# Optimization experiments

Measured on AMD Instinct MI355X. Metric: run time of the kernel, lower is better.

Reference implementation:

```python
import jax, jax.numpy as jnp
import numpy as np

B, U, D, H = 8, 256, 512, 32

def _layernorm(x, g, b, eps=1e-5):
    m = jnp.mean(x, axis=-1, keepdims=True)
    v = jnp.var(x, axis=-1, keepdims=True)
    return (x - m) * jax.lax.rsqrt(v + eps) * g + b

def setup_inputs() -> dict:
    key = jax.random.key(0)
    ks = jax.random.split(key, 12)
    s = 0.02
    return {
        "z_dyn": jax.random.normal(ks[0], (B, U, D), jnp.float32),
        "z_sem": jax.random.normal(ks[1], (B, U, D), jnp.float32),
        "te_w": jax.random.normal(ks[2], (H, D), jnp.float32) * s,
        "w_ih": jax.random.normal(ks[3], (3 * D, D), jnp.float32) * s,
        "w_hh": jax.random.normal(ks[4], (3 * D, D), jnp.float32) * s,
        "b_ih": jnp.zeros((3 * D,), jnp.float32),
        "b_hh": jnp.zeros((3 * D,), jnp.float32),
        "ln_g": jnp.ones((D,), jnp.float32),
        "ln_b": jnp.zeros((D,), jnp.float32),
        "ln2_g": jnp.ones((2 * D,), jnp.float32),
        "ln2_b": jnp.zeros((2 * D,), jnp.float32),
        "w1": jax.random.normal(ks[5], (D, 2 * D), jnp.float32) * s,
        "b1": jnp.zeros((D,), jnp.float32),
        "w2": jax.random.normal(ks[6], (D, D), jnp.float32) * s,
        "b2": jnp.zeros((D,), jnp.float32),
        "horizon": H,
    }

def reference(z_dyn, z_sem, te_w, w_ih, w_hh, b_ih, b_hh, ln_g, ln_b,
              ln2_g, ln2_b, w1, b1, w2, b2, horizon):
    b, u, d = z_dyn.shape
    h0 = z_dyn.reshape(b * u, d)
    sem = z_sem.reshape(b * u, d)
    idx = jnp.minimum(jnp.arange(horizon), te_w.shape[0] - 1)
    ts = te_w[idx]  # [horizon, d]

    def step(h, t):
        x = sem + t
        gi = x @ w_ih.T + b_ih   # [bu, 3d]
        gh = h @ w_hh.T + b_hh
        ir, iz, inn = jnp.split(gi, 3, axis=-1)
        hr, hz, hn = jnp.split(gh, 3, axis=-1)
        r = jax.nn.sigmoid(ir + hr)
        z = jax.nn.sigmoid(iz + hz)
        n = jnp.tanh(inn + r * hn)
        h_new = (1.0 - z) * n + z * h
        h_norm = _layernorm(h_new, ln_g, ln_b)
        cat = jnp.concatenate([sem, h_norm], axis=-1)
        hid = jax.nn.gelu(_layernorm(cat, ln2_g, ln2_b) @ w1.T + b1,
                          approximate=False)
        sem_h = sem + hid @ w2.T + b2
        return h_new, (h_norm, sem_h)

    _, (dyn, sems) = jax.lax.scan(step, h0, ts)  # [horizon, bu, d]
    dyn = dyn.reshape(horizon, b, u, d).transpose(1, 2, 0, 3)
    sems = sems.reshape(horizon, b, u, d).transpose(1, 2, 0, 3)
    return dyn, sems
```

## Files before the change

kernel.cpp:

```cpp
#include <hip/hip_runtime.h>
#include <math.h>


typedef unsigned short u16;
using bf16x8 = __attribute__((ext_vector_type(8))) short;
using f32x4  = __attribute__((ext_vector_type(4))) float;

#define DEV __device__ __forceinline__

constexpr int D   = 512;
constexpr int D3  = 1536;
constexpr int H   = 32;
constexpr int BU  = 2048;
constexpr long long OUT_HALF = (long long)BU * H * D;

DEV u16 f2bf(float x){
  union { float f; unsigned u; } c; c.f = x;
  unsigned u = c.u;
  u += 0x7fffu + ((u >> 16) & 1u);
  return (u16)(u >> 16);
}
DEV float bf2f(u16 b){
  union { unsigned u; float f; } c; c.u = ((unsigned)b) << 16; return c.f;
}

DEV void gload_lds16(const void* g, void* l){
  __builtin_amdgcn_global_load_lds(
      (const __attribute__((address_space(1))) void*)g,
      (__attribute__((address_space(3))) void*)l, 16, 0, 0);
}

DEV f32x4 mfma16(bf16x8 a, bf16x8 b, f32x4 c){
  return __builtin_amdgcn_mfma_f32_16x16x32_bf16(a, b, c, 0, 0, 0);
}

DEV float fsigm(float x){ return 1.f / (1.f + __expf(-x)); }
DEV float ftanh(float x){ return 1.f - 2.f / (1.f + __expf(2.f * x)); }

__global__ __launch_bounds__(256) void prep_kernel(
    const float* __restrict__ z_dyn, const float* __restrict__ z_sem,
    const float* __restrict__ te_w,  const float* __restrict__ w_ih,
    const float* __restrict__ w_hh,  const float* __restrict__ ln_g,
    const float* __restrict__ ln_b,  const float* __restrict__ ln2_g,
    const float* __restrict__ ln2_b, const float* __restrict__ w1,
    const float* __restrict__ b1,    const float* __restrict__ w2,
    float* __restrict__ h1, u16* __restrict__ hbh2, u16* __restrict__ hbl2,
    u16* __restrict__ sem_hi, u16* __restrict__ sem_lo,
    u16* __restrict__ wih_hi, u16* __restrict__ wih_lo,
    u16* __restrict__ whh_hi, u16* __restrict__ whh_lo,
    u16* __restrict__ W1s, u16* __restrict__ W1g, u16* __restrict__ w2bf,
    float* __restrict__ c1, float* __restrict__ c2p,
    float* __restrict__ d1, float* __restrict__ d2, float* __restrict__ Tg)
{
  int i = blockIdx.x * 256 + threadIdx.x;
  if (i < BU * D) {
    float hv = z_dyn[i];
    h1[i] = hv;
    u16 hh = f2bf(hv);
    hbh2[i] = hh;
    hbl2[i] = f2bf(hv - bf2f(hh));
    float sv = z_sem[i];
    u16 sh_ = f2bf(sv);
    sem_hi[i] = sh_;
    sem_lo[i] = f2bf(sv - bf2f(sh_));
  }
  if (i < D3 * D) {
    float wv = w_ih[i];
    u16 wh = f2bf(wv);
    wih_hi[i] = wh;
    wih_lo[i] = f2bf(wv - bf2f(wh));
    float uv = w_hh[i];
    u16 uh = f2bf(uv);
    whh_hi[i] = uh;
    whh_lo[i] = f2bf(uv - bf2f(uh));
  }
  if (i < D * D) {
    int k = i >> 9, j = i & 511;
    W1s[i]  = f2bf(w1[k * 1024 + j] * ln2_g[j]);
    w2bf[i] = f2bf(w2[i]);
  }
  if (i < D * 64) {
    int r = i >> 6, ln = i & 63;
    float sc1 = 0.f, sc2 = 0.f, sd1 = 0.f, sd2 = 0.f;
    #pragma unroll
    for (int jj = 0; jj < 8; ++jj) {
      int j = jj * 64 + ln;
      float wA = w1[r * 1024 + j];
      float wB = w1[r * 1024 + 512 + j];
      sc1 += wA * ln2_g[j] + wB * ln2_g[512 + j];
      sc2 += wA * ln2_b[j] + wB * ln2_b[512 + j];
      float wBg = wB * ln2_g[512 + j];
      float wg = wBg * ln_g[j];
      sd1 += wg;
      sd2 += wBg * ln_b[j];
      W1g[r * 512 + j] = f2bf(wg);
    }
    #pragma unroll
    for (int o = 1; o < 64; o <<= 1) {
      sc1 += __shfl_xor(sc1, o); sc2 += __shfl_xor(sc2, o);
      sd1 += __shfl_xor(sd1, o); sd2 += __shfl_xor(sd2, o);
    }
    if (ln == 0) {
      c1[r] = sc1;
      c2p[r] = sc2 + b1[r];
      d1[r] = sd1;
      d2[r] = sd2;
    }
  }
  if (i < H * D3) {
    int c = i >> 5, t = i & 31;
    float s = 0.f;
    for (int d0 = 0; d0 < D; ++d0) s += te_w[t * D + d0] * w_ih[c * D + d0];
    Tg[t * D3 + c] = s;
  }
}

__global__ __launch_bounds__(256) void rowstats_kernel(
    const float* __restrict__ sem, float* __restrict__ Ssem,
    float* __restrict__ Ssem2)
{
  const int wid = threadIdx.x >> 6, lane = threadIdx.x & 63;
  const int row = blockIdx.x * 4 + wid;
  const float* p = sem + (size_t)row * D + lane * 8;
  float4 a0 = *(const float4*)p;
  float4 a1 = *(const float4*)(p + 4);
  float s  = a0.x + a0.y + a0.z + a0.w + a1.x + a1.y + a1.z + a1.w;
  float s2 = a0.x*a0.x + a0.y*a0.y + a0.z*a0.z + a0.w*a0.w
           + a1.x*a1.x + a1.y*a1.y + a1.z*a1.z + a1.w*a1.w;
  #pragma unroll
  for (int o = 1; o < 64; o <<= 1) { s += __shfl_xor(s, o); s2 += __shfl_xor(s2, o); }
  if (lane == 0) { Ssem[row] = s; Ssem2[row] = s2; }
}

__global__ __launch_bounds__(256) void setup_kernel(
    const u16* __restrict__ sem_hi, const u16* __restrict__ sem_lo,
    const u16* __restrict__ wih_hi, const u16* __restrict__ wih_lo,
    const u16* __restrict__ W1s, float* __restrict__ G0,
    float* __restrict__ Psem, const float* __restrict__ b_ih)
{
  __shared__ __align__(16) char smem[32768];
  char* Ah = smem;
  char* Al = smem + 8192;
  char* Bh = smem + 16384;
  char* Bl = smem + 24576;
  const int tid = threadIdx.x, wid = tid >> 6, lane = tid & 63;
  const int wr = wid >> 1, wc = wid & 1;
  const bool isG0 = blockIdx.y < 24;
  const u16* Bsrc = isG0 ? wih_hi : W1s;
  const int row0 = blockIdx.x * 64;
  const int col0 = (isG0 ? blockIdx.y : blockIdx.y - 24) * 64;

  f32x4 acc[2][2] = {};
  for (int kt = 0; kt < 8; ++kt) {
    #pragma unroll
    for (int it = 0; it < 2; ++it) {
      int s = it * 256 + tid, pr = s >> 3, pc = s & 7;
      int lch = pc ^ (pr & 7);
      size_t aoff = (size_t)(row0 + pr) * D + kt * 64 + lch * 8;
      size_t boff = (size_t)(col0 + pr) * D + kt * 64 + lch * 8;
      gload_lds16(sem_hi + aoff, Ah + it * 4096 + wid * 1024);
      gload_lds16(Bsrc + boff,   Bh + it * 4096 + wid * 1024);
      if (isG0) {
        gload_lds16(sem_lo + aoff, Al + it * 4096 + wid * 1024);
        gload_lds16(wih_lo + boff, Bl + it * 4096 + wid * 1024);
      }
    }
    asm volatile("s_waitcnt vmcnt(0)" ::: "memory");
    __syncthreads();

    const int lc = lane & 15, hi2 = lane >> 4;
    #pragma unroll
    for (int kk = 0; kk < 2; ++kk) {
      int ch = kk * 4 + hi2;
      bf16x8 afh[2], afl[2], bfh[2], bfl[2];
      #pragma unroll
      for (int mi = 0; mi < 2; ++mi) {
        int r = wr * 32 + mi * 16 + lc;
        int o = r * 128 + ((ch ^ (r & 7)) << 4);
        afh[mi] = *(const bf16x8*)(Ah + o);
        if (isG0) afl[mi] = *(const bf16x8*)(Al + o);
      }
      #pragma unroll
      for (int ci = 0; ci < 2; ++ci) {
        int r = wc * 32 + ci * 16 + lc;
        int o = r * 128 + ((ch ^ (r & 7)) << 4);
        bfh[ci] = *(const bf16x8*)(Bh + o);
        if (isG0) bfl[ci] = *(const bf16x8*)(Bl + o);
      }
      #pragma unroll
      for (int mi = 0; mi < 2; ++mi)
        #pragma unroll
        for (int ci = 0; ci < 2; ++ci) {
          f32x4 a = acc[mi][ci];
          a = mfma16(afh[mi], bfh[ci], a);
          if (isG0) {
            a = mfma16(afl[mi], bfh[ci], a);
            a = mfma16(afh[mi], bfl[ci], a);
          }
          acc[mi][ci] = a;
        }
    }
    __syncthreads();
  }
  const int lj = lane >> 4, lc2 = lane & 15;
  #pragma unroll
  for (int mi = 0; mi < 2; ++mi)
    #pragma unroll
    for (int ci = 0; ci < 2; ++ci)
      #pragma unroll
      for (int j = 0; j < 4; ++j) {
        int row = row0 + wr * 32 + mi * 16 + lj * 4 + j;
        int col = col0 + wc * 32 + ci * 16 + lc2;
        float v = acc[mi][ci][j];
        if (isG0) G0[(size_t)row * D3 + col] = v + b_ih[col];
        else      Psem[(size_t)row * D + col] = v;
      }
}

__global__ __launch_bounds__(256, 4) void fused_kernel(
    int t,
    const u16* __restrict__ hbh_in, const u16* __restrict__ hbl_in,
    u16* __restrict__ hbh_out, u16* __restrict__ hbl_out,
    const float* __restrict__ hf_in, float* __restrict__ hf_out,
    const u16* __restrict__ whh_hi, const u16* __restrict__ whh_lo,
    const float* __restrict__ G0, const float* __restrict__ Tg,
    const float* __restrict__ bhh,
    float4* __restrict__ stats_w, float* __restrict__ dyn,
    const float* __restrict__ ln_g, const float* __restrict__ ln_b,
    const float* __restrict__ Ssem, const float* __restrict__ Ssem2,
    const u16* __restrict__ lbh,
    const float4* __restrict__ stats_r, const u16* __restrict__ W1g,
    const float* __restrict__ Psem, const float* __restrict__ d1,
    const float* __restrict__ d2, const float* __restrict__ c1,
    const float* __restrict__ c2p, u16* __restrict__ hid_w,
    const u16* __restrict__ hid_r, const u16* __restrict__ w2bf,
    const float* __restrict__ zsem, const float* __restrict__ b2,
    float* __restrict__ sems)
{
  __shared__ __align__(16) char smem[32768];
  const int bid = blockIdx.x;
  const int tid = threadIdx.x, wid = tid >> 6, lane = tid & 63;
  const int wr = wid >> 1, wc = wid & 1;
  const int lc = lane & 15, hi2 = lane >> 4;
  const int lj = lane >> 4, lc2 = lane & 15;

  if (bid < 512) {
    if (t >= H) return;
    const int row0 = (bid & 31) * 64;
    const int gc   = (bid >> 5) * 32;
    char* Ah = smem;
    char* Al = smem + 8192;
    char* Bh = smem + 16384;
    char* Bl = smem + 28672;
    f32x4 acc[3][2] = {};

    const int gcol = gc + wc * 16 + lc2;

    float pre_gr[2][4], pre_gz[2][4], pre_gn[2][4], pre_hf[2][4];
    #pragma unroll
    for (int mi = 0; mi < 2; ++mi)
      #pragma unroll
      for (int j = 0; j < 4; ++j) {
        int row = row0 + wr * 32 + mi * 16 + lj * 4 + j;
        size_t g0i = (size_t)row * D3 + gcol;
        pre_gr[mi][j] = G0[g0i];
        pre_gz[mi][j] = G0[g0i + 512];
        pre_gn[mi][j] = G0[g0i + 1024];
        pre_hf[mi][j] = hf_in[(size_t)row * D + gcol];
      }

    for (int kt = 0; kt < 8; ++kt) {
      #pragma unroll
      for (int it = 0; it < 2; ++it) {
        int s = it * 256 + tid, pr = s >> 3, pc = s & 7;
        int lch = pc ^ (pr & 7);
        size_t off = (size_t)(row0 + pr) * D + kt * 64 + lch * 8;
        gload_lds16(hbh_in + off, Ah + it * 4096 + wid * 1024);
        gload_lds16(hbl_in + off, Al + it * 4096 + wid * 1024);
      }
      #pragma unroll
      for (int it = 0; it < 3; ++it) {
        int s = it * 256 + tid, pr = s >> 3, pc = s & 7;
        int lch = pc ^ (pr & 7);
        int g = pr >> 5, lr = pr & 31;
        gload_lds16(whh_hi + (size_t)(g * D + gc + lr) * D + kt * 64 + lch * 8,
                    Bh + it * 4096 + wid * 1024);
      }
      {
        int pr = tid >> 3, pc = tid & 7;
        int lch = pc ^ (pr & 7);
        gload_lds16(whh_lo + (size_t)(2 * D + gc + pr) * D + kt * 64 + lch * 8,
                    Bl + wid * 1024);
      }
      asm volatile("s_waitcnt vmcnt(0)" ::: "memory");
      __syncthreads();

      #pragma unroll
      for (int kk = 0; kk < 2; ++kk) {
        int ch = kk * 4 + hi2;
        bf16x8 afh[2], afl[2];
        #pragma unroll
        for (int mi = 0; mi < 2; ++mi) {
          int r = wr * 32 + mi * 16 + lc;
          int o = r * 128 + ((ch ^ (r & 7)) << 4);
          afh[mi] = *(const bf16x8*)(Ah + o);
          afl[mi] = *(const bf16x8*)(Al + o);
        }
        const int rloc = wc * 16 + lc;
        #pragma unroll
        for (int g = 0; g < 3; ++g) {
          int rb = g * 32 + rloc;
          int bo = rb * 128 + ((ch ^ (rb & 7)) << 4);
          bf16x8 bh = *(const bf16x8*)(Bh + bo);
          #pragma unroll
          for (int mi = 0; mi < 2; ++mi) {
            f32x4 a = acc[g][mi];
            a = mfma16(afh[mi], bh, a);
            a = mfma16(afl[mi], bh, a);
            acc[g][mi] = a;
          }
        }
        {
          int bo = rloc * 128 + ((ch ^ (rloc & 7)) << 4);
          bf16x8 bl = *(const bf16x8*)(Bl + bo);
          #pragma unroll
          for (int mi = 0; mi < 2; ++mi)
            acc[2][mi] = mfma16(afh[mi], bl, acc[2][mi]);
        }
      }
      __syncthreads();
    }

    const float br = bhh[gcol];
    const float bz = bhh[512 + gcol];
    const float bn = bhh[1024 + gcol];
    const float tr = Tg[t * D3 + gcol];
    const float tz = Tg[t * D3 + 512 + gcol];
    const float tn = Tg[t * D3 + 1024 + gcol];
    #pragma unroll
    for (int mi = 0; mi < 2; ++mi)
      #pragma unroll
      for (int j = 0; j < 4; ++j) {
        int row = row0 + wr * 32 + mi * 16 + lj * 4 + j;
        float gr = pre_gr[mi][j] + tr + acc[0][mi][j];
        float gz = pre_gz[mi][j] + tz + acc[1][mi][j];
        float gn = pre_gn[mi][j] + tn;
        float r = fsigm(gr + br);
        float z = fsigm(gz + bz);
        float n = ftanh(gn + r * (acc[2][mi][j] + bn));
        size_t hi_ = (size_t)row * D + gcol;
        float hnew = (1.f - z) * n + z * pre_hf[mi][j];
        hf_out[hi_] = hnew;
        u16 hh = f2bf(hnew);
        hbh_out[hi_] = hh;
        hbl_out[hi_] = f2bf(hnew - bf2f(hh));
      }
  } else if (bid < 768) {
    if (t < 2 || t > H + 1) return;
    const int i = bid - 512;
    const int row0 = (i & 31) * 64, col0 = (i >> 5) * 64;
    char* bufp[2] = { smem, smem + 16384 };
    f32x4 acc[2][2] = {};

    float pre_ps[2][2][4];
    float4 pre_st[2][4];
    #pragma unroll
    for (int mi = 0; mi < 2; ++mi)
      #pragma unroll
      for (int j = 0; j < 4; ++j) {
        int row = row0 + wr * 32 + mi * 16 + lj * 4 + j;
        pre_st[mi][j] = stats_r[row];
        #pragma unroll
        for (int ci = 0; ci < 2; ++ci) {
          int col = col0 + wc * 32 + ci * 16 + lc2;
          pre_ps[mi][ci][j] = Psem[(size_t)row * D + col];
        }
      }

    auto stage = [&](char* base, int kt){
      #pragma unroll
      for (int it = 0; it < 2; ++it) {
        int s = it * 256 + tid, pr = s >> 3, pc = s & 7;
        int lch = pc ^ (pr & 7);
        gload_lds16(lbh + (size_t)(row0 + pr) * D + kt * 64 + lch * 8,
                    base + it * 4096 + wid * 1024);
        gload_lds16(W1g + (size_t)(col0 + pr) * D + kt * 64 + lch * 8,
                    base + 8192 + it * 4096 + wid * 1024);
      }
    };

    stage(bufp[0], 0);
    __syncthreads();
    int buf = 0;
    for (int kt = 0; kt < 8; ++kt) {
      if (kt < 7) stage(bufp[buf ^ 1], kt + 1);
      const char* Ah = bufp[buf];
      const char* Bs = bufp[buf] + 8192;
      #pragma unroll
      for (int kk = 0; kk < 2; ++kk) {
        int ch = kk * 4 + hi2;
        bf16x8 afh[2], bf[2];
        #pragma unroll
        for (int mi = 0; mi < 2; ++mi) {
          int r = wr * 32 + mi * 16 + lc;
          afh[mi] = *(const bf16x8*)(Ah + r * 128 + ((ch ^ (r & 7)) << 4));
        }
        #pragma unroll
        for (int ci = 0; ci < 2; ++ci) {
          int r = wc * 32 + ci * 16 + lc;
          bf[ci] = *(const bf16x8*)(Bs + r * 128 + ((ch ^ (r & 7)) << 4));
        }
        #pragma unroll
        for (int mi = 0; mi < 2; ++mi)
          #pragma unroll
          for (int ci = 0; ci < 2; ++ci)
            acc[mi][ci] = mfma16(afh[mi], bf[ci], acc[mi][ci]);
      }
      __syncthreads();
      buf ^= 1;
    }

    #pragma unroll
    for (int mi = 0; mi < 2; ++mi)
      #pragma unroll
      for (int ci = 0; ci < 2; ++ci)
        #pragma unroll
        for (int j = 0; j < 4; ++j) {
          int row = row0 + wr * 32 + mi * 16 + lj * 4 + j;
          int col = col0 + wc * 32 + ci * 16 + lc2;
          float4 st = pre_st[mi][j];
          float hn_w1 = st.x * acc[mi][ci][j] - st.y * d1[col] + d2[col];
          float pre = st.z * (pre_ps[mi][ci][j] + hn_w1)
                      - st.w * c1[col] + c2p[col];
          float gl = 0.5f * pre * (1.f + erff(pre * 0.70710678118654752f));
          hid_w[(size_t)row * D + col] = f2bf(gl);
        }
  } else if (bid < 1024) {
    if (t < 3) return;
    const int ts = t - 3;
    const int i = bid - 768;
    const int row0 = (i & 31) * 64, col0 = (i >> 5) * 64;
    char* bufp[2] = { smem, smem + 16384 };
    f32x4 acc[2][2] = {};

    float pre_zs[2][2][4];
    #pragma unroll
    for (int mi = 0; mi < 2; ++mi)
      #pragma unroll
      for (int ci = 0; ci < 2; ++ci)
        #pragma unroll
        for (int j = 0; j < 4; ++j) {
          int row = row0 + wr * 32 + mi * 16 + lj * 4 + j;
          int col = col0 + wc * 32 + ci * 16 + lc2;
          pre_zs[mi][ci][j] = zsem[(size_t)row * D + col];
        }

    auto stage = [&](char* base, int kt){
      #pragma unroll
      for (int it = 0; it < 2; ++it) {
        int s = it * 256 + tid, pr = s >> 3, pc = s & 7;
        int lch = pc ^ (pr & 7);
        gload_lds16(hid_r + (size_t)(row0 + pr) * D + kt * 64 + lch * 8,
                    base + it * 4096 + wid * 1024);
        gload_lds16(w2bf + (size_t)(col0 + pr) * D + kt * 64 + lch * 8,
                    base + 8192 + it * 4096 + wid * 1024);
      }
    };

    stage(bufp[0], 0);
    __syncthreads();
    int buf = 0;
    for (int kt = 0; kt < 8; ++kt) {
      if (kt < 7) stage(bufp[buf ^ 1], kt + 1);
      const char* As = bufp[buf];
      const char* Bs = bufp[buf] + 8192;
      #pragma unroll
      for (int kk = 0; kk < 2; ++kk) {
        int ch = kk * 4 + hi2;
        bf16x8 af[2], bf[2];
        #pragma unroll
        for (int mi = 0; mi < 2; ++mi) {
          int r = wr * 32 + mi * 16 + lc;
          af[mi] = *(const bf16x8*)(As + r * 128 + ((ch ^ (r & 7)) << 4));
        }
        #pragma unroll
        for (int ci = 0; ci < 2; ++ci) {
          int r = wc * 32 + ci * 16 + lc;
          bf[ci] = *(const bf16x8*)(Bs + r * 128 + ((ch ^ (r & 7)) << 4));
        }
        #pragma unroll
        for (int mi = 0; mi < 2; ++mi)
          #pragma unroll
          for (int ci = 0; ci < 2; ++ci)
            acc[mi][ci] = mfma16(af[mi], bf[ci], acc[mi][ci]);
      }
      __syncthreads();
      buf ^= 1;
    }

    #pragma unroll
    for (int mi = 0; mi < 2; ++mi)
      #pragma unroll
      for (int ci = 0; ci < 2; ++ci)
        #pragma unroll
        for (int j = 0; j < 4; ++j) {
          int row = row0 + wr * 32 + mi * 16 + lj * 4 + j;
          int col = col0 + wc * 32 + ci * 16 + lc2;
          float v = pre_zs[mi][ci][j] + acc[mi][ci][j] + b2[col];
          __builtin_nontemporal_store(
              v, &sems[((size_t)row * H + ts) * D + col]);
        }
  } else {
    if (t < 1 || t > H) return;
    const int tt = t - 1;
    const int base = (bid - 1024) * 16 + wid * 4;
    const float4 g0 = *(const float4*)(ln_g + lane * 8);
    const float4 g1 = *(const float4*)(ln_g + lane * 8 + 4);
    const float4 b0 = *(const float4*)(ln_b + lane * 8);
    const float4 b1v = *(const float4*)(ln_b + lane * 8 + 4);
    const float gg[8] = {g0.x,g0.y,g0.z,g0.w,g1.x,g1.y,g1.z,g1.w};
    const float bb[8] = {b0.x,b0.y,b0.z,b0.w,b1v.x,b1v.y,b1v.z,b1v.w};

    for (int rr = 0; rr < 4; ++rr) {
      const int row = base + rr;
      const float* hp = hf_in + (size_t)row * D + lane * 8;
      float4 a0 = *(const float4*)hp, a1 = *(const float4*)(hp + 4);
      float h[8] = {a0.x, a0.y, a0.z, a0.w, a1.x, a1.y, a1.z, a1.w};
      float s1 = 0.f;
      #pragma unroll
      for (int k = 0; k < 8; ++k) s1 += h[k];
      #pragma unroll
      for (int o = 1; o < 64; o <<= 1) s1 += __shfl_xor(s1, o);
      float m1 = s1 * (1.f / 512.f);
      float s2 = 0.f;
      #pragma unroll
      for (int k = 0; k < 8; ++k) {
        float dv = h[k] - m1;
        s2 += dv * dv;
      }
      #pragma unroll
      for (int o = 1; o < 64; o <<= 1) s2 += __shfl_xor(s2, o);
      float rsd1 = rsqrtf(s2 * (1.f / 512.f) + 1e-5f);

      float hn[8];
      float sh = 0.f, sh2 = 0.f;
      #pragma unroll
      for (int k = 0; k < 8; ++k) {
        float x = (h[k] - m1) * rsd1 * gg[k] + bb[k];
        hn[k] = x; sh += x; sh2 += x * x;
      }
      float* dp = dyn + ((size_t)row * H + tt) * D + lane * 8;
      f32x4 v0 = {hn[0], hn[1], hn[2], hn[3]};
      f32x4 v1 = {hn[4], hn[5], hn[6], hn[7]};
      __builtin_nontemporal_store(v0, (f32x4*)dp);
      __builtin_nontemporal_store(v1, (f32x4*)(dp + 4));

      #pragma unroll
      for (int o = 1; o < 64; o <<= 1) {
        sh += __shfl_xor(sh, o); sh2 += __shfl_xor(sh2, o);
      }
      if (lane == 0) {
        float m2 = (Ssem[row] + sh) * (1.f / 1024.f);
        float vv = (Ssem2[row] + sh2) * (1.f / 1024.f) - m2 * m2;
        float rs2 = rsqrtf(vv + 1e-5f);
        stats_w[row] = make_float4(rsd1, m1 * rsd1, rs2, m2 * rs2);
      }
    }
  }
}

extern "C" void kernel_launch(void* const* d_in, const int* in_sizes, int n_in,
                              void* d_out, int out_size, void* d_ws, size_t ws_size,
                              hipStream_t stream)
{
  (void)in_sizes; (void)n_in; (void)out_size; (void)ws_size;
  const float* z_dyn = (const float*)d_in[0];
  const float* z_sem = (const float*)d_in[1];
  const float* te_w  = (const float*)d_in[2];
  const float* w_ih  = (const float*)d_in[3];
  const float* w_hh  = (const float*)d_in[4];
  const float* b_ih  = (const float*)d_in[5];
  const float* b_hh  = (const float*)d_in[6];
  const float* ln_g  = (const float*)d_in[7];
  const float* ln_b  = (const float*)d_in[8];
  const float* ln2_g = (const float*)d_in[9];
  const float* ln2_b = (const float*)d_in[10];
  const float* w1    = (const float*)d_in[11];
  const float* b1    = (const float*)d_in[12];
  const float* w2    = (const float*)d_in[13];
  const float* b2    = (const float*)d_in[14];

  char* ws = (char*)d_ws;
  const size_t MB = 1ull << 20;
  u16* hbh[3] = { (u16*)(ws + 0),      (u16*)(ws + 2 * MB),  (u16*)(ws + 4 * MB) };
  u16* hbl[3] = { (u16*)(ws + 6 * MB), (u16*)(ws + 8 * MB),  (u16*)(ws + 10 * MB) };
  float* G0     = (float*)(ws + 12 * MB);
  float* Psem   = (float*)(ws + 25 * MB);
  u16*  sem_hi  = (u16*)(ws + 29 * MB);
  u16*  sem_lo  = (u16*)(ws + 31 * MB);
  u16*  hid0    = (u16*)(ws + 33 * MB);
  u16*  hid1    = (u16*)(ws + 35 * MB);
  u16*  wih_hi  = (u16*)(ws + 37 * MB);
  u16*  wih_lo  = (u16*)(ws + 37 * MB + 1572864);
  u16*  whh_hi  = (u16*)(ws + 40 * MB);
  u16*  whh_lo  = (u16*)(ws + 40 * MB + 1572864);
  u16*  W1s     = (u16*)(ws + 43 * MB);
  u16*  W1g     = (u16*)(ws + 43 * MB + 524288);
  u16*  w2bf    = (u16*)(ws + 44 * MB);
  float* c1     = (float*)(ws + 45 * MB);
  float* c2p    = (float*)(ws + 45 * MB + 16384);
  float* d1     = (float*)(ws + 45 * MB + 32768);
  float* d2     = (float*)(ws + 45 * MB + 49152);
  float* Ssem   = (float*)(ws + 45 * MB + 65536);
  float* Ssem2  = (float*)(ws + 45 * MB + 81920);
  float4* stats0 = (float4*)(ws + 46 * MB);
  float4* stats1 = (float4*)(ws + 46 * MB + 32768);
  float* Tg     = (float*)(ws + 47 * MB);
  float* hf0    = (float*)(ws + 48 * MB);
  float* hf1    = (float*)(ws + 52 * MB);

  float* outp = (float*)d_out;
  float* out_dyn  = outp;
  float* out_sems = outp + OUT_HALF;

  prep_kernel<<<4096, 256, 0, stream>>>(
      z_dyn, z_sem, te_w, w_ih, w_hh, ln_g, ln_b, ln2_g, ln2_b, w1, b1, w2,
      hf1, hbh[2], hbl[2], sem_hi, sem_lo, wih_hi, wih_lo, whh_hi, whh_lo,
      W1s, W1g, w2bf, c1, c2p, d1, d2, Tg);
  rowstats_kernel<<<512, 256, 0, stream>>>(z_sem, Ssem, Ssem2);
  setup_kernel<<<dim3(32, 32), 256, 0, stream>>>(
      sem_hi, sem_lo, wih_hi, wih_lo, W1s, G0, Psem, b_ih);

  for (int t = 0; t <= H + 2; ++t) {
    int s_out  = ((t % 3) + 3) % 3;
    int s_in   = (((t - 1) % 3) + 3) % 3;
    int s_ln   = (((t - 2) % 3) + 3) % 3;
    float* hf_out      = (t & 1) ? hf1 : hf0;
    const float* hf_in = (t & 1) ? hf0 : hf1;
    float4* st_w = ((t - 1) & 1) ? stats1 : stats0;
    const float4* st_r = ((t - 2) & 1) ? stats1 : stats0;
    u16* hidw = ((t - 2) & 1) ? hid1 : hid0;
    const u16* hidr = ((t - 3) & 1) ? hid1 : hid0;

    fused_kernel<<<dim3(1152), dim3(256), 0, stream>>>(
        t,
        hbh[s_in], hbl[s_in], hbh[s_out], hbl[s_out],
        hf_in, hf_out,
        whh_hi, whh_lo, G0, Tg, b_hh,
        st_w, out_dyn, ln_g, ln_b, Ssem, Ssem2,
        hbh[s_ln], st_r, W1g, Psem, d1, d2, c1, c2p, hidw,
        hidr, w2bf, z_sem, b2, out_sems);
  }
}
```

Before: 722.4 us.

## Double-buffer the recurrent GEMM K-loop with async LDS prefetch

Splits the K loop of the hidden-state GEMM into 16 steps of 32 columns and alternates between two 16KB LDS buffers. The loads for step kt+2 are issued right after step kt's compute, and a partial vmcnt wait lets global loads overlap MFMA work. The swizzle is reworked to fit the 64-byte row halves. This costs twice as many barriers and smaller per-step compute, and it depends on vmcnt counting being exact.

```diff
diff --git a/kernel.cpp b/kernel.cpp
--- a/kernel.cpp
+++ b/kernel.cpp
@@ -248,10 +248,8 @@
     if (t >= H) return;
     const int row0 = (bid & 31) * 64;
     const int gc   = (bid >> 5) * 32;
-    char* Ah = smem;
-    char* Al = smem + 8192;
-    char* Bh = smem + 16384;
-    char* Bl = smem + 28672;
+    char* b0 = smem;
+    char* b1 = smem + 16384;
     f32x4 acc[3][2] = {};
 
     const int gcol = gc + wc * 16 + lc2;
@@ -269,66 +267,72 @@
         pre_hf[mi][j] = hf_in[(size_t)row * D + gcol];
       }
 
-    for (int kt = 0; kt < 8; ++kt) {
+    auto stage = [&](char* base, int kt){
+      { int row = tid >> 2;
+        int ko = kt * 32 + (((tid & 3) ^ ((tid >> 3) & 3)) << 3);
+        size_t off = (size_t)(row0 + row) * D + ko;
+        gload_lds16(hbh_in + off, base + wid * 1024);
+        gload_lds16(hbl_in + off, base + 4096 + wid * 1024);
+      }
       #pragma unroll
       for (int it = 0; it < 2; ++it) {
-        int s = it * 256 + tid, pr = s >> 3, pc = s & 7;
-        int lch = pc ^ (pr & 7);
-        size_t off = (size_t)(row0 + pr) * D + kt * 64 + lch * 8;
-        gload_lds16(hbh_in + off, Ah + it * 4096 + wid * 1024);
-        gload_lds16(hbl_in + off, Al + it * 4096 + wid * 1024);
-      }
-      #pragma unroll
-      for (int it = 0; it < 3; ++it) {
-        int s = it * 256 + tid, pr = s >> 3, pc = s & 7;
-        int lch = pc ^ (pr & 7);
-        int g = pr >> 5, lr = pr & 31;
-        gload_lds16(whh_hi + (size_t)(g * D + gc + lr) * D + kt * 64 + lch * 8,
-                    Bh + it * 4096 + wid * 1024);
-      }
-      {
-        int pr = tid >> 3, pc = tid & 7;
-        int lch = pc ^ (pr & 7);
-        gload_lds16(whh_lo + (size_t)(2 * D + gc + pr) * D + kt * 64 + lch * 8,
-                    Bl + wid * 1024);
-      }
-      asm volatile("s_waitcnt vmcnt(0)" ::: "memory");
-      __syncthreads();
-
-      #pragma unroll
-      for (int kk = 0; kk < 2; ++kk) {
-        int ch = kk * 4 + hi2;
-        bf16x8 afh[2], afl[2];
+        int s = it * 256 + tid;
+        int row = s >> 2;
+        int ko = kt * 32 + (((s & 3) ^ ((s >> 3) & 3)) << 3);
+        const u16* src = (row < 96)
+            ? whh_hi + (size_t)((row >> 5) * D + gc + (row & 31)) * D + ko
+            : whh_lo + (size_t)(2 * D + gc + (row & 31)) * D + ko;
+        gload_lds16(src, base + 8192 + it * 4096 + wid * 1024);
+      }
+    };
+
+    auto compute = [&](const char* base){
+      const int ch = hi2;
+      bf16x8 afh[2], afl[2];
+      #pragma unroll
+      for (int mi = 0; mi < 2; ++mi) {
+        int ra = wr * 32 + mi * 16 + lc;
+        int ao = (ra >> 1) * 128 + (ra & 1) * 64
+               + ((ch ^ ((ra >> 1) & 3)) << 4);
+        afh[mi] = *(const bf16x8*)(base + ao);
+        afl[mi] = *(const bf16x8*)(base + 4096 + ao);
+      }
+      const int rloc = wc * 16 + lc;
+      #pragma unroll
+      for (int g = 0; g < 3; ++g) {
+        int rb = g * 32 + rloc;
+        int bo = (rb >> 1) * 128 + (rb & 1) * 64
+               + ((ch ^ ((rb >> 1) & 3)) << 4);
+        bf16x8 bh = *(const bf16x8*)(base + 8192 + bo);
         #pragma unroll
         for (int mi = 0; mi < 2; ++mi) {
-          int r = wr * 32 + mi * 16 + lc;
-          int o = r * 128 + ((ch ^ (r & 7)) << 4);
-          afh[mi] = *(const bf16x8*)(Ah + o);
-          afl[mi] = *(const bf16x8*)(Al + o);
-        }
-        const int rloc = wc * 16 + lc;
-        #pragma unroll
-        for (int g = 0; g < 3; ++g) {
-          int rb = g * 32 + rloc;
-          int bo = rb * 128 + ((ch ^ (rb & 7)) << 4);
-          bf16x8 bh = *(const bf16x8*)(Bh + bo);
-          #pragma unroll
-          for (int mi = 0; mi < 2; ++mi) {
-            f32x4 a = acc[g][mi];
-            a = mfma16(afh[mi], bh, a);
-            a = mfma16(afl[mi], bh, a);
-            acc[g][mi] = a;
-          }
-        }
-        {
-          int bo = rloc * 128 + ((ch ^ (rloc & 7)) << 4);
-          bf16x8 bl = *(const bf16x8*)(Bl + bo);
-          #pragma unroll
-          for (int mi = 0; mi < 2; ++mi)
-            acc[2][mi] = mfma16(afh[mi], bl, acc[2][mi]);
-        }
-      }
-      __syncthreads();
+          f32x4 a = acc[g][mi];
+          a = mfma16(afh[mi], bh, a);
+          a = mfma16(afl[mi], bh, a);
+          acc[g][mi] = a;
+        }
+      }
+      { int rb = 96 + rloc;
+        int bo = (rb >> 1) * 128 + (rb & 1) * 64
+               + ((ch ^ ((rb >> 1) & 3)) << 4);
+        bf16x8 bl = *(const bf16x8*)(base + 8192 + bo);
+        #pragma unroll
+        for (int mi = 0; mi < 2; ++mi)
+          acc[2][mi] = mfma16(afh[mi], bl, acc[2][mi]);
+      }
+    };
+
+    stage(b0, 0);
+    stage(b1, 1);
+    int buf = 0;
+    for (int kt = 0; kt < 16; ++kt) {
+      if (kt == 15) asm volatile("s_waitcnt vmcnt(0)" ::: "memory");
+      else          asm volatile("s_waitcnt vmcnt(4)" ::: "memory");
+      __builtin_amdgcn_s_barrier();
+      compute(buf ? b1 : b0);
+      __builtin_amdgcn_s_barrier();
+      if (kt < 14) stage(buf ? b1 : b0, kt + 2);
+      buf ^= 1;
     }
 
     const float br = bhh[gcol];
```

After: 769.6 us. 6.5% more time.
